# Optimization experiments

Hardware: AMD Instinct MI355X
Metric: run time of the kernel (lower is better)

## Reference

```python
import jax, jax.numpy as jnp
import numpy as np

N = 30000
E = 300000
DIN, DH, DOUT, L = 256, 128, 64, 6


def setup_inputs() -> dict:
    key = jax.random.key(0)
    ks = jax.random.split(key, 8)
    feats = jax.random.normal(ks[0], (N, DIN), dtype=jnp.float32)
    src = jax.random.randint(ks[1], (E,), 0, N, dtype=jnp.int32)
    dst = jax.random.randint(ks[2], (E,), 0, N, dtype=jnp.int32)
    W0 = jax.random.normal(ks[3], (DIN, DH), dtype=jnp.float32) * 0.05
    b0 = jnp.zeros((DH,), dtype=jnp.float32)
    Wh = jax.random.normal(ks[4], (L, DH, DH), dtype=jnp.float32) * 0.05
    bh = jnp.zeros((L, DH), dtype=jnp.float32)
    Wout = jax.random.normal(ks[5], (DH * (L + 1), DOUT), dtype=jnp.float32) * 0.05
    bout = jnp.zeros((DOUT,), dtype=jnp.float32)
    return {"feats": feats, "src": src, "dst": dst, "W0": W0, "b0": b0,
            "Wh": Wh, "bh": bh, "Wout": Wout, "bout": bout}


def _graph_conv(x, W, b, src, dst, inv_sqrt_out, inv_sqrt_in):
    # DGL GraphConv, norm='both': D_out^{-1/2} -> sum over edges -> D_in^{-1/2} -> XW+b -> relu
    x = x * inv_sqrt_out[:, None]
    m = jax.ops.segment_sum(x[src], dst, num_segments=N)  # [N, d]
    m = m * inv_sqrt_in[:, None]
    return jax.nn.relu(m @ W + b)


def reference(feats, src, dst, W0, b0, Wh, bh, Wout, bout):
    ones = jnp.ones((E,), dtype=jnp.float32)
    out_deg = jax.ops.segment_sum(ones, src, num_segments=N)
    in_deg = jax.ops.segment_sum(ones, dst, num_segments=N)
    inv_sqrt_out = jax.lax.rsqrt(jnp.clip(out_deg, 1.0))
    inv_sqrt_in = jax.lax.rsqrt(jnp.clip(in_deg, 1.0))

    h = _graph_conv(feats, W0, b0, src, dst, inv_sqrt_out, inv_sqrt_in)
    reps = [h]
    for i in range(L):
        h = _graph_conv(h, Wh[i], bh[i], src, dst, inv_sqrt_out, inv_sqrt_in)
        reps.append(h)
    jk = jnp.concatenate(reps, axis=-1)  # [N, DH*(L+1)]
    # update_all(copy_u, sum): un-normalized neighborhood sum
    h = jax.ops.segment_sum(jk[src], dst, num_segments=N)
    return h @ Wout + bout
```

## Files before the change

kernel.cpp:

```cpp
#include <hip/hip_runtime.h>

#define NN 30000
#define NE 300000
#define D_IN 256
#define D_H 128
#define D_OUT 64
#define NL 6

typedef unsigned short ushort_t;
typedef unsigned int uint_t;
typedef __attribute__((ext_vector_type(8))) short sh8;
typedef __attribute__((ext_vector_type(4))) float f4;

static __device__ __forceinline__ ushort_t f2bf(float f) {
    uint_t u = __float_as_uint(f);
    u = (u + 0x7FFFu + ((u >> 16) & 1u)) >> 16;
    return (ushort_t)u;
}

__global__ void degree_kernel(const int* __restrict__ src, const int* __restrict__ dst,
                              int* __restrict__ outdeg, int* __restrict__ indeg) {
    int e = blockIdx.x * blockDim.x + threadIdx.x;
    if (e < NE) {
        atomicAdd(&outdeg[src[e]], 1);
        atomicAdd(&indeg[dst[e]], 1);
    }
}

__global__ void rsqrt_kernel(const int* __restrict__ deg, float* __restrict__ inv, int n) {
    int i = blockIdx.x * blockDim.x + threadIdx.x;
    if (i < n) {
        float d = (float)deg[i];
        inv[i] = rsqrtf(d < 1.0f ? 1.0f : d);
    }
}

__global__ __launch_bounds__(1024) void scan_kernel(const int* __restrict__ deg,
                                                    int* __restrict__ row_ptr) {
    __shared__ int wsum[16];
    __shared__ int chunk_base;
    if (threadIdx.x == 0) chunk_base = 0;
    __syncthreads();
    const int lane = threadIdx.x & 63;
    const int wid = threadIdx.x >> 6;
    for (int base = 0; base < NN; base += 1024) {
        int i = base + threadIdx.x;
        int v = (i < NN) ? deg[i] : 0;
        int s = v;
#pragma unroll
        for (int off = 1; off < 64; off <<= 1) {
            int t = __shfl_up(s, off, 64);
            if (lane >= off) s += t;
        }
        if (lane == 63) wsum[wid] = s;
        __syncthreads();
        if (wid == 0 && lane < 16) {
            int ws = wsum[lane];
#pragma unroll
            for (int off = 1; off < 16; off <<= 1) {
                int t = __shfl_up(ws, off, 64);
                if (lane >= off) ws += t;
            }
            wsum[lane] = ws;
        }
        __syncthreads();
        int cb = chunk_base;
        int woff = (wid > 0) ? wsum[wid - 1] : 0;
        if (i < NN) row_ptr[i] = cb + woff + s - v;
        int total = wsum[15];
        __syncthreads();
        if (threadIdx.x == 0) chunk_base = cb + total;
        __syncthreads();
    }
    if (threadIdx.x == 0) row_ptr[NN] = chunk_base;
}

__global__ void fill_kernel(const int* __restrict__ src, const int* __restrict__ dst,
                            const int* __restrict__ row_ptr, int* __restrict__ cursor,
                            int* __restrict__ col) {
    int e = blockIdx.x * blockDim.x + threadIdx.x;
    if (e < NE) {
        int d = dst[e];
        int pos = atomicAdd(&cursor[d], 1);
        col[row_ptr[d] + pos] = src[e];
    }
}

__global__ void featconv_kernel(const float* __restrict__ F, ushort_t* __restrict__ Fb) {
    int i = blockIdx.x * blockDim.x + threadIdx.x;
    if (i >= NN * D_IN / 8) return;
    float4 a = *(const float4*)(F + (size_t)i * 8);
    float4 b = *(const float4*)(F + (size_t)i * 8 + 4);
    uint4 o;
    o.x = (uint_t)f2bf(a.x) | ((uint_t)f2bf(a.y) << 16);
    o.y = (uint_t)f2bf(a.z) | ((uint_t)f2bf(a.w) << 16);
    o.z = (uint_t)f2bf(b.x) | ((uint_t)f2bf(b.y) << 16);
    o.w = (uint_t)f2bf(b.z) | ((uint_t)f2bf(b.w) << 16);
    *(uint4*)(Fb + (size_t)i * 8) = o;
}

__global__ void packw_kernel(const float* __restrict__ W0,
                             const float* __restrict__ Wh,
                             const float* __restrict__ Wout,
                             ushort_t* __restrict__ W0p,
                             ushort_t* __restrict__ Whp,
                             ushort_t* __restrict__ Woutp) {
    int g = blockIdx.x * blockDim.x + threadIdx.x;
    int frag = g >> 6;
    int lane = g & 63;
    if (frag >= 368) return;
    const float* srcw;
    ushort_t* dstp;
    int fl, KF, M;
    if (frag < 64) {
        fl = frag; KF = 8; M = 128;
        srcw = W0;
        dstp = W0p;
    } else if (frag < 64 + 192) {
        int f2 = frag - 64;
        int l = f2 / 32; fl = f2 % 32; KF = 4; M = 128;
        srcw = Wh + (size_t)l * D_H * D_H;
        dstp = Whp + (size_t)l * 32 * 512;
    } else {
        int f2 = frag - 256;
        int l = f2 / 16; fl = f2 % 16; KF = 4; M = 64;
        srcw = Wout + (size_t)l * D_H * D_OUT;
        dstp = Woutp + (size_t)l * 16 * 512;
    }
    int ct = fl / KF;
    int kt = fl % KF;
    int krow = kt * 32 + (lane >> 4) * 8;
    int cidx = ct * 16 + (lane & 15);
    ushort_t tmp[8];
#pragma unroll
    for (int j = 0; j < 8; j++)
        tmp[j] = f2bf(srcw[(size_t)(krow + j) * M + cidx]);
    uint4 o;
    o.x = (uint_t)tmp[0] | ((uint_t)tmp[1] << 16);
    o.y = (uint_t)tmp[2] | ((uint_t)tmp[3] << 16);
    o.z = (uint_t)tmp[4] | ((uint_t)tmp[5] << 16);
    o.w = (uint_t)tmp[6] | ((uint_t)tmp[7] << 16);
    *(uint4*)(dstp + (size_t)fl * 512 + lane * 8) = o;
}

template <int KF, bool HAS_T, bool HAS_P>
__global__ __launch_bounds__(256) void gemm_mfma(
    const ushort_t* __restrict__ Xb,
    const ushort_t* __restrict__ W1p,
    const ushort_t* __restrict__ W2p,
    const float* __restrict__ scale,
    ushort_t* __restrict__ Tb,
    float* __restrict__ P,
    int nrows)
{
    constexpr int K = KF * 32;
    const int lane = threadIdx.x & 63;
    const int w = threadIdx.x >> 6;
    const int rg = w >> 1;
    const int cgrp = w & 1;
    const int row0 = blockIdx.x * 32 + rg * 16;

    int arow = row0 + (lane & 15);
    if (arow >= nrows) arow = nrows - 1;
    const ushort_t* xr = Xb + (size_t)arow * K + ((lane >> 4) * 8);
    sh8 a[KF];
#pragma unroll
    for (int kt = 0; kt < KF; kt++)
        a[kt] = *(const sh8*)(xr + kt * 32);

    const int crow0 = row0 + (lane >> 4) * 4;

    if (HAS_T) {
        float s[4];
#pragma unroll
        for (int r = 0; r < 4; r++) {
            int rw = crow0 + r;
            s[r] = scale[rw < nrows ? rw : nrows - 1];
        }
#pragma unroll
        for (int i = 0; i < 4; i++) {
            int ct = cgrp * 4 + i;
            f4 acc = {0.f, 0.f, 0.f, 0.f};
            const ushort_t* wp = W1p + ((size_t)(ct * KF) << 9) + lane * 8;
#pragma unroll
            for (int kt = 0; kt < KF; kt++)
                acc = __builtin_amdgcn_mfma_f32_16x16x32_bf16(
                    a[kt], *(const sh8*)(wp + ((size_t)kt << 9)), acc, 0, 0, 0);
            int colb = ct * 16 + (lane & 15);
#pragma unroll
            for (int r = 0; r < 4; r++) {
                int rw = crow0 + r;
                if (rw < nrows)
                    Tb[(size_t)rw * 128 + colb] = f2bf(acc[r] * s[r]);
            }
        }
    }
    if (HAS_P) {
#pragma unroll
        for (int i = 0; i < 2; i++) {
            int ct = cgrp * 2 + i;
            f4 acc = {0.f, 0.f, 0.f, 0.f};
            const ushort_t* wp = W2p + ((size_t)(ct * KF) << 9) + lane * 8;
#pragma unroll
            for (int kt = 0; kt < KF; kt++)
                acc = __builtin_amdgcn_mfma_f32_16x16x32_bf16(
                    a[kt], *(const sh8*)(wp + ((size_t)kt << 9)), acc, 0, 0, 0);
            int colb = ct * 16 + (lane & 15);
#pragma unroll
            for (int r = 0; r < 4; r++) {
                int rw = crow0 + r;
                if (rw < nrows) {
                    float* pp = P + (size_t)rw * 64 + colb;
                    *pp += acc[r];
                }
            }
        }
    }
}

__global__ __launch_bounds__(256) void gather_bf16_kernel(
    const ushort_t* __restrict__ Tb,
    const int* __restrict__ row_ptr,
    const int* __restrict__ col,
    const float* __restrict__ scale,
    const float* __restrict__ bias,
    ushort_t* __restrict__ Yb) {
    int idx = blockIdx.x * blockDim.x + threadIdx.x;
    int node = idx >> 4;
    int q = idx & 15;
    if (node >= NN) return;
    int beg = row_ptr[node];
    int end = row_ptr[node + 1];
    const uint_t* T32 = (const uint_t*)Tb;
    float acc[8];
#pragma unroll
    for (int i = 0; i < 8; i++) acc[i] = 0.f;

    int j = beg;
    for (; j + 3 < end; j += 4) {
        int c0 = col[j], c1 = col[j + 1], c2 = col[j + 2], c3 = col[j + 3];
        uint4 u0 = *(const uint4*)(T32 + (size_t)c0 * 64 + q * 4);
        uint4 u1 = *(const uint4*)(T32 + (size_t)c1 * 64 + q * 4);
        uint4 u2 = *(const uint4*)(T32 + (size_t)c2 * 64 + q * 4);
        uint4 u3 = *(const uint4*)(T32 + (size_t)c3 * 64 + q * 4);
        uint_t w0[4] = {u0.x, u0.y, u0.z, u0.w};
        uint_t w1[4] = {u1.x, u1.y, u1.z, u1.w};
        uint_t w2[4] = {u2.x, u2.y, u2.z, u2.w};
        uint_t w3[4] = {u3.x, u3.y, u3.z, u3.w};
#pragma unroll
        for (int i = 0; i < 4; i++) {
            acc[2 * i] += (__uint_as_float(w0[i] << 16) + __uint_as_float(w1[i] << 16))
                        + (__uint_as_float(w2[i] << 16) + __uint_as_float(w3[i] << 16));
            acc[2 * i + 1] += (__uint_as_float(w0[i] & 0xFFFF0000u) + __uint_as_float(w1[i] & 0xFFFF0000u))
                            + (__uint_as_float(w2[i] & 0xFFFF0000u) + __uint_as_float(w3[i] & 0xFFFF0000u));
        }
    }
    for (; j < end; j++) {
        int c0 = col[j];
        uint4 u0 = *(const uint4*)(T32 + (size_t)c0 * 64 + q * 4);
        uint_t w0[4] = {u0.x, u0.y, u0.z, u0.w};
#pragma unroll
        for (int i = 0; i < 4; i++) {
            acc[2 * i]     += __uint_as_float(w0[i] << 16);
            acc[2 * i + 1] += __uint_as_float(w0[i] & 0xFFFF0000u);
        }
    }

    float s = scale[node];
    float h[8];
#pragma unroll
    for (int i = 0; i < 8; i++)
        h[i] = fmaxf(fmaf(acc[i], s, bias[q * 8 + i]), 0.f);
    uint4 o;
    o.x = (uint_t)f2bf(h[0]) | ((uint_t)f2bf(h[1]) << 16);
    o.y = (uint_t)f2bf(h[2]) | ((uint_t)f2bf(h[3]) << 16);
    o.z = (uint_t)f2bf(h[4]) | ((uint_t)f2bf(h[5]) << 16);
    o.w = (uint_t)f2bf(h[6]) | ((uint_t)f2bf(h[7]) << 16);
    *(uint4*)(Yb + (size_t)node * 128 + q * 8) = o;
}

__global__ __launch_bounds__(256) void gather_f32_kernel(
    const float* __restrict__ P,
    const int* __restrict__ row_ptr,
    const int* __restrict__ col,
    const float* __restrict__ bias,
    float* __restrict__ Y) {
    int idx = blockIdx.x * blockDim.x + threadIdx.x;
    int node = idx >> 4;
    int q = idx & 15;
    if (node >= NN) return;
    int beg = row_ptr[node];
    int end = row_ptr[node + 1];
    float4 acc = make_float4(0.f, 0.f, 0.f, 0.f);
    int j = beg;
    for (; j + 3 < end; j += 4) {
        int c0 = col[j], c1 = col[j + 1], c2 = col[j + 2], c3 = col[j + 3];
        float4 v0 = *(const float4*)(P + (size_t)c0 * 64 + q * 4);
        float4 v1 = *(const float4*)(P + (size_t)c1 * 64 + q * 4);
        float4 v2 = *(const float4*)(P + (size_t)c2 * 64 + q * 4);
        float4 v3 = *(const float4*)(P + (size_t)c3 * 64 + q * 4);
        acc.x += (v0.x + v1.x) + (v2.x + v3.x);
        acc.y += (v0.y + v1.y) + (v2.y + v3.y);
        acc.z += (v0.z + v1.z) + (v2.z + v3.z);
        acc.w += (v0.w + v1.w) + (v2.w + v3.w);
    }
    for (; j < end; j++) {
        int c0 = col[j];
        float4 v0 = *(const float4*)(P + (size_t)c0 * 64 + q * 4);
        acc.x += v0.x; acc.y += v0.y; acc.z += v0.z; acc.w += v0.w;
    }
    float4 b = *(const float4*)(bias + q * 4);
    acc.x += b.x; acc.y += b.y; acc.z += b.z; acc.w += b.w;
    *(float4*)(Y + (size_t)node * 64 + q * 4) = acc;
}

extern "C" void kernel_launch(void* const* d_in, const int* in_sizes, int n_in,
                              void* d_out, int out_size, void* d_ws, size_t ws_size,
                              hipStream_t stream) {
    const float* feats = (const float*)d_in[0];
    const int*   src   = (const int*)d_in[1];
    const int*   dst   = (const int*)d_in[2];
    const float* W0    = (const float*)d_in[3];
    const float* b0    = (const float*)d_in[4];
    const float* Wh    = (const float*)d_in[5];
    const float* bh    = (const float*)d_in[6];
    const float* Wout  = (const float*)d_in[7];
    const float* bout  = (const float*)d_in[8];
    float* out = (float*)d_out;

    float* ws      = (float*)d_ws;
    float* inv_out = ws;
    float* inv_in  = ws + NN;
    float* p       = ws + 2 * NN;
    ushort_t* tb   = (ushort_t*)(p + (size_t)NN * 64);
    ushort_t* ha   = tb + (size_t)NN * 128;
    ushort_t* hb   = ha + (size_t)NN * 128;
    ushort_t* fb   = hb + (size_t)NN * 128;
    ushort_t* w0p  = fb + (size_t)NN * 256;
    ushort_t* whp  = w0p + 64 * 512;
    ushort_t* wop  = whp + 192 * 512;
    int* ibase     = (int*)(wop + 112 * 512);
    int* outdeg_i  = ibase;
    int* indeg_i   = ibase + NN;
    int* row_ptr   = ibase + 2 * NN;
    int* cursor    = ibase + 3 * NN + 1;
    int* col       = ibase + 4 * NN + 1;

    const int B = 256;
    const int gemm_blocks = (NN + 31) / 32;
    const int gather_blocks = (NN * 16 + B - 1) / B;

    hipMemsetAsync(outdeg_i, 0, 2 * NN * sizeof(int), stream);
    hipMemsetAsync(cursor, 0, NN * sizeof(int), stream);
    hipMemsetAsync(p, 0, (size_t)NN * D_OUT * sizeof(float), stream);
    degree_kernel<<<(NE + B - 1) / B, B, 0, stream>>>(src, dst, outdeg_i, indeg_i);
    rsqrt_kernel<<<(2 * NN + B - 1) / B, B, 0, stream>>>(outdeg_i, inv_out, 2 * NN);
    scan_kernel<<<1, 1024, 0, stream>>>(indeg_i, row_ptr);
    fill_kernel<<<(NE + B - 1) / B, B, 0, stream>>>(src, dst, row_ptr, cursor, col);
    featconv_kernel<<<(NN * D_IN / 8 + B - 1) / B, B, 0, stream>>>(feats, fb);
    packw_kernel<<<(368 * 64 + B - 1) / B, B, 0, stream>>>(W0, Wh, Wout, w0p, whp, wop);

    gemm_mfma<8, true, false><<<gemm_blocks, 256, 0, stream>>>(
        fb, w0p, nullptr, inv_out, tb, nullptr, NN);
    gather_bf16_kernel<<<gather_blocks, B, 0, stream>>>(
        tb, row_ptr, col, inv_in, b0, ha);

    ushort_t* hcur = ha;
    ushort_t* hnext = hb;
    for (int l = 0; l < NL; l++) {
        gemm_mfma<4, true, true><<<gemm_blocks, 256, 0, stream>>>(
            hcur, whp + (size_t)l * 32 * 512, wop + (size_t)l * 16 * 512,
            inv_out, tb, p, NN);
        gather_bf16_kernel<<<gather_blocks, B, 0, stream>>>(
            tb, row_ptr, col, inv_in, bh + (size_t)l * D_H, hnext);
        ushort_t* tmp = hcur; hcur = hnext; hnext = tmp;
    }

    gemm_mfma<4, false, true><<<gemm_blocks, 256, 0, stream>>>(
        hcur, nullptr, wop + (size_t)NL * 16 * 512, nullptr, nullptr, p, NN);

    gather_f32_kernel<<<gather_blocks, B, 0, stream>>>(p, row_ptr, col, bout, out);
}
```

Measured before the change: 376.2 us.

## Sort CSR columns by source via two-pass fill and gather output in bf16

CSR construction now first buckets edges by source (a second scan plus fill1), then scatters them into destination rows (fill2). Within each row the column indices therefore come out roughly sorted by source, which should make neighbour gathers more cache-local in every layer. The final projection is converted to bf16 by a new pconv kernel, so the output gather reads half the bytes. This adds a scan, a fill pass and a conversion kernel, and rounding the final sum inputs to bf16 adds precision loss.

```diff
diff --git a/kernel.cpp b/kernel.cpp
--- a/kernel.cpp
+++ b/kernel.cpp
@@ -36,7 +36,7 @@
 }
 
 __global__ __launch_bounds__(1024) void scan_kernel(const int* __restrict__ deg,
-                                                    int* __restrict__ row_ptr) {
+                                                    int* __restrict__ ptr) {
     __shared__ int wsum[16];
     __shared__ int chunk_base;
     if (threadIdx.x == 0) chunk_base = 0;
@@ -66,23 +66,34 @@
         __syncthreads();
         int cb = chunk_base;
         int woff = (wid > 0) ? wsum[wid - 1] : 0;
-        if (i < NN) row_ptr[i] = cb + woff + s - v;
+        if (i < NN) ptr[i] = cb + woff + s - v;
         int total = wsum[15];
         __syncthreads();
         if (threadIdx.x == 0) chunk_base = cb + total;
         __syncthreads();
     }
-    if (threadIdx.x == 0) row_ptr[NN] = chunk_base;
-}
-
-__global__ void fill_kernel(const int* __restrict__ src, const int* __restrict__ dst,
-                            const int* __restrict__ row_ptr, int* __restrict__ cursor,
-                            int* __restrict__ col) {
+    if (threadIdx.x == 0) ptr[NN] = chunk_base;
+}
+
+__global__ void fill1_kernel(const int* __restrict__ src, const int* __restrict__ dst,
+                             const int* __restrict__ src_ptr, int* __restrict__ scur,
+                             int2* __restrict__ es) {
     int e = blockIdx.x * blockDim.x + threadIdx.x;
     if (e < NE) {
-        int d = dst[e];
-        int pos = atomicAdd(&cursor[d], 1);
-        col[row_ptr[d] + pos] = src[e];
+        int s = src[e];
+        int pos = atomicAdd(&scur[s], 1);
+        es[src_ptr[s] + pos] = make_int2(s, dst[e]);
+    }
+}
+
+__global__ void fill2_kernel(const int2* __restrict__ es,
+                             const int* __restrict__ row_ptr, int* __restrict__ cursor,
+                             int* __restrict__ col) {
+    int i = blockIdx.x * blockDim.x + threadIdx.x;
+    if (i < NE) {
+        int2 e = es[i];
+        int pos = atomicAdd(&cursor[e.y], 1);
+        col[row_ptr[e.y] + pos] = e.x;
     }
 }
 
@@ -97,6 +108,19 @@
     o.z = (uint_t)f2bf(b.x) | ((uint_t)f2bf(b.y) << 16);
     o.w = (uint_t)f2bf(b.z) | ((uint_t)f2bf(b.w) << 16);
     *(uint4*)(Fb + (size_t)i * 8) = o;
+}
+
+__global__ void pconv_kernel(const float* __restrict__ P, ushort_t* __restrict__ Pb) {
+    int i = blockIdx.x * blockDim.x + threadIdx.x;
+    if (i >= NN * D_OUT / 8) return;
+    float4 a = *(const float4*)(P + (size_t)i * 8);
+    float4 b = *(const float4*)(P + (size_t)i * 8 + 4);
+    uint4 o;
+    o.x = (uint_t)f2bf(a.x) | ((uint_t)f2bf(a.y) << 16);
+    o.y = (uint_t)f2bf(a.z) | ((uint_t)f2bf(a.w) << 16);
+    o.z = (uint_t)f2bf(b.x) | ((uint_t)f2bf(b.y) << 16);
+    o.w = (uint_t)f2bf(b.z) | ((uint_t)f2bf(b.w) << 16);
+    *(uint4*)(Pb + (size_t)i * 8) = o;
 }
 
 __global__ void packw_kernel(const float* __restrict__ W0,
@@ -279,39 +303,64 @@
     *(uint4*)(Yb + (size_t)node * 128 + q * 8) = o;
 }
 
-__global__ __launch_bounds__(256) void gather_f32_kernel(
-    const float* __restrict__ P,
+__global__ __launch_bounds__(256) void gather_out_kernel(
+    const ushort_t* __restrict__ Pb,
     const int* __restrict__ row_ptr,
     const int* __restrict__ col,
     const float* __restrict__ bias,
     float* __restrict__ Y) {
     int idx = blockIdx.x * blockDim.x + threadIdx.x;
-    int node = idx >> 4;
-    int q = idx & 15;
+    int node = idx >> 3;
+    int q = idx & 7;
     if (node >= NN) return;
     int beg = row_ptr[node];
     int end = row_ptr[node + 1];
-    float4 acc = make_float4(0.f, 0.f, 0.f, 0.f);
+    const uint_t* P32 = (const uint_t*)Pb;
+    float acc[8];
+#pragma unroll
+    for (int i = 0; i < 8; i++) acc[i] = 0.f;
+
     int j = beg;
     for (; j + 3 < end; j += 4) {
         int c0 = col[j], c1 = col[j + 1], c2 = col[j + 2], c3 = col[j + 3];
-        float4 v0 = *(const float4*)(P + (size_t)c0 * 64 + q * 4);
-        float4 v1 = *(const float4*)(P + (size_t)c1 * 64 + q * 4);
-        float4 v2 = *(const float4*)(P + (size_t)c2 * 64 + q * 4);
-        float4 v3 = *(const float4*)(P + (size_t)c3 * 64 + q * 4);
-        acc.x += (v0.x + v1.x) + (v2.x + v3.x);
-        acc.y += (v0.y + v1.y) + (v2.y + v3.y);
-        acc.z += (v0.z + v1.z) + (v2.z + v3.z);
-        acc.w += (v0.w + v1.w) + (v2.w + v3.w);
+        uint4 u0 = *(const uint4*)(P32 + (size_t)c0 * 32 + q * 4);
+        uint4 u1 = *(const uint4*)(P32 + (size_t)c1 * 32 + q * 4);
+        uint4 u2 = *(const uint4*)(P32 + (size_t)c2 * 32 + q * 4);
+        uint4 u3 = *(const uint4*)(P32 + (size_t)c3 * 32 + q * 4);
+        uint_t w0[4] = {u0.x, u0.y, u0.z, u0.w};
+        uint_t w1[4] = {u1.x, u1.y, u1.z, u1.w};
+        uint_t w2[4] = {u2.x, u2.y, u2.z, u2.w};
+        uint_t w3[4] = {u3.x, u3.y, u3.z, u3.w};
+#pragma unroll
+        for (int i = 0; i < 4; i++) {
+            acc[2 * i] += (__uint_as_float(w0[i] << 16) + __uint_as_float(w1[i] << 16))
+                        + (__uint_as_float(w2[i] << 16) + __uint_as_float(w3[i] << 16));
+            acc[2 * i + 1] += (__uint_as_float(w0[i] & 0xFFFF0000u) + __uint_as_float(w1[i] & 0xFFFF0000u))
+                            + (__uint_as_float(w2[i] & 0xFFFF0000u) + __uint_as_float(w3[i] & 0xFFFF0000u));
+        }
     }
     for (; j < end; j++) {
         int c0 = col[j];
-        float4 v0 = *(const float4*)(P + (size_t)c0 * 64 + q * 4);
-        acc.x += v0.x; acc.y += v0.y; acc.z += v0.z; acc.w += v0.w;
-    }
-    float4 b = *(const float4*)(bias + q * 4);
-    acc.x += b.x; acc.y += b.y; acc.z += b.z; acc.w += b.w;
-    *(float4*)(Y + (size_t)node * 64 + q * 4) = acc;
+        uint4 u0 = *(const uint4*)(P32 + (size_t)c0 * 32 + q * 4);
+        uint_t w0[4] = {u0.x, u0.y, u0.z, u0.w};
+#pragma unroll
+        for (int i = 0; i < 4; i++) {
+            acc[2 * i]     += __uint_as_float(w0[i] << 16);
+            acc[2 * i + 1] += __uint_as_float(w0[i] & 0xFFFF0000u);
+        }
+    }
+
+    float4 o0, o1;
+    o0.x = acc[0] + bias[q * 8 + 0];
+    o0.y = acc[1] + bias[q * 8 + 1];
+    o0.z = acc[2] + bias[q * 8 + 2];
+    o0.w = acc[3] + bias[q * 8 + 3];
+    o1.x = acc[4] + bias[q * 8 + 4];
+    o1.y = acc[5] + bias[q * 8 + 5];
+    o1.z = acc[6] + bias[q * 8 + 6];
+    o1.w = acc[7] + bias[q * 8 + 7];
+    *(float4*)(Y + (size_t)node * 64 + q * 8) = o0;
+    *(float4*)(Y + (size_t)node * 64 + q * 8 + 4) = o1;
 }
 
 extern "C" void kernel_launch(void* const* d_in, const int* in_sizes, int n_in,
@@ -336,27 +385,34 @@
     ushort_t* ha   = tb + (size_t)NN * 128;
     ushort_t* hb   = ha + (size_t)NN * 128;
     ushort_t* fb   = hb + (size_t)NN * 128;
-    ushort_t* w0p  = fb + (size_t)NN * 256;
+    ushort_t* pb   = fb + (size_t)NN * 256;
+    ushort_t* w0p  = pb + (size_t)NN * 64;
     ushort_t* whp  = w0p + 64 * 512;
     ushort_t* wop  = whp + 192 * 512;
     int* ibase     = (int*)(wop + 112 * 512);
     int* outdeg_i  = ibase;
     int* indeg_i   = ibase + NN;
     int* row_ptr   = ibase + 2 * NN;
-    int* cursor    = ibase + 3 * NN + 1;
-    int* col       = ibase + 4 * NN + 1;
+    int* src_ptr   = row_ptr + NN + 1;
+    int* cursor    = src_ptr + NN + 1;
+    int* scur      = cursor + NN;
+    int* col       = scur + NN;
+    int2* es       = (int2*)(col + NE);
 
     const int B = 256;
     const int gemm_blocks = (NN + 31) / 32;
     const int gather_blocks = (NN * 16 + B - 1) / B;
+    const int gout_blocks = (NN * 8 + B - 1) / B;
 
     hipMemsetAsync(outdeg_i, 0, 2 * NN * sizeof(int), stream);
-    hipMemsetAsync(cursor, 0, NN * sizeof(int), stream);
+    hipMemsetAsync(cursor, 0, 2 * NN * sizeof(int), stream);
     hipMemsetAsync(p, 0, (size_t)NN * D_OUT * sizeof(float), stream);
     degree_kernel<<<(NE + B - 1) / B, B, 0, stream>>>(src, dst, outdeg_i, indeg_i);
     rsqrt_kernel<<<(2 * NN + B - 1) / B, B, 0, stream>>>(outdeg_i, inv_out, 2 * NN);
     scan_kernel<<<1, 1024, 0, stream>>>(indeg_i, row_ptr);
-    fill_kernel<<<(NE + B - 1) / B, B, 0, stream>>>(src, dst, row_ptr, cursor, col);
+    scan_kernel<<<1, 1024, 0, stream>>>(outdeg_i, src_ptr);
+    fill1_kernel<<<(NE + B - 1) / B, B, 0, stream>>>(src, dst, src_ptr, scur, es);
+    fill2_kernel<<<(NE + B - 1) / B, B, 0, stream>>>(es, row_ptr, cursor, col);
     featconv_kernel<<<(NN * D_IN / 8 + B - 1) / B, B, 0, stream>>>(feats, fb);
     packw_kernel<<<(368 * 64 + B - 1) / B, B, 0, stream>>>(W0, Wh, Wout, w0p, whp, wop);
 
@@ -379,5 +435,6 @@
     gemm_mfma<4, false, true><<<gemm_blocks, 256, 0, stream>>>(
         hcur, nullptr, wop + (size_t)NL * 16 * 512, nullptr, nullptr, p, NN);
 
-    gather_f32_kernel<<<gather_blocks, B, 0, stream>>>(p, row_ptr, col, bout, out);
-}
+    pconv_kernel<<<(NN * D_OUT / 8 + B - 1) / B, B, 0, stream>>>(p, pb);
+    gather_out_kernel<<<gout_blocks, B, 0, stream>>>(pb, row_ptr, col, bout, out);
+}
```

After: 419.3 us. 11.5% more time.
